# Kernel optimization log

Measured on AMD Instinct MI355X. Metric: run time of the kernel, lower is better.

Reference implementation:

```python
import jax, jax.numpy as jnp
import numpy as np

B, D, OUT, K = 2048, 256, 256, 16


def setup_inputs() -> dict:
    key = jax.random.key(0)
    k1, k2, k3, k4 = jax.random.split(key, 4)
    x = jax.random.normal(k1, (B, D), dtype=jnp.float32)
    values = jax.random.uniform(k2, (OUT, D, K), dtype=jnp.float32, minval=-0.05, maxval=0.05)
    skip_w = jax.random.normal(k3, (OUT, D), dtype=jnp.float32) * (1.0 / np.sqrt(D).astype(np.float32))
    skip_b = jax.random.normal(k4, (OUT,), dtype=jnp.float32) * 0.01
    return {"x": x, "values": values, "skip_w": skip_w, "skip_b": skip_b}


def reference(x, values, skip_w, skip_b):
    # x: (B, D); values: (OUT, D, K); skip_w: (OUT, D); skip_b: (OUT,)
    num_knots = values.shape[-1]
    grid = jnp.linspace(-1.0, 1.0, num_knots)  # (K,)
    xc = jnp.clip(x, -1.0, 1.0)
    # torch.bucketize(x, grid) with right=False == searchsorted side='left'
    right = jnp.searchsorted(grid, xc, side='left')
    left = jnp.clip(right - 1, 0, num_knots - 2)  # (B, D)
    right = left + 1
    g0 = grid[left]
    g1 = grid[right]
    w = (xc - g0) / (g1 - g0 + 1e-12)  # (B, D)
    # Gather spline values per (sample, input-dim) knot bucket.
    vt = jnp.transpose(values, (1, 2, 0))  # (D, K, OUT)
    dim_idx = jnp.arange(xc.shape[1])[None, :]  # (1, D)
    v_left = vt[dim_idx, left]    # (B, D, OUT)
    v_right = vt[dim_idx, right]  # (B, D, OUT)
    # Linear interpolation + sum over input dims.
    y = jnp.sum((1.0 - w)[..., None] * v_left + w[..., None] * v_right, axis=1)  # (B, OUT)
    # Skip connection on the clamped input (torch reassigns x = clamp(x) first).
    return y + xc @ skip_w.T + skip_b
```

## Files before the change

### kernel.cpp

```cpp
#include <hip/hip_runtime.h>
#include <hip/hip_bf16.h>


namespace {
constexpr int Bsz  = 2048;
constexpr int Din  = 256;
constexpr int Dout = 256;
constexpr int Kn   = 16;
constexpr int KKNOT = Din * Kn;
constexpr int Ksp   = KKNOT + Din;
constexpr int KB    = Ksp / 32;
constexpr int KBK   = KKNOT / 32;
constexpr float INV_H = 7.5f;
constexpr float Hgrid = 2.0f / 15.0f;

constexpr int NSPLIT = 9;
constexpr int STK    = 8;
constexpr int STS    = 4;
constexpr int PELEM  = Bsz * Dout;
constexpr int SXS    = 36;
}

typedef __attribute__((ext_vector_type(8))) short shortx8;
typedef __attribute__((ext_vector_type(4))) float floatx4;

__device__ __forceinline__ unsigned int f2bf(float f) {
  __hip_bfloat16 h = __float2bfloat16(f);
  return (unsigned int)*reinterpret_cast<unsigned short*>(&h);
}
__device__ __forceinline__ float clamp1(float v) {
  return fminf(1.f, fmaxf(-1.f, v));
}
__device__ __forceinline__ unsigned int packbf(unsigned int e0, unsigned int e1) {
  return (e1 & 0xffff0000u) | (e0 >> 16);
}
__device__ __forceinline__ unsigned int rnd(float f) {
  return __float_as_uint(f) + 0x8000u;
}

__global__ __launch_bounds__(256) void kan_prep(
    const float* __restrict__ values, const float* __restrict__ skip_w,
    unsigned short* __restrict__ Wf) {
  const int tid = blockIdx.x * 256 + threadIdx.x;
  const int q  = tid & 3;
  const int n  = (tid >> 2) & 15;
  const int og = (tid >> 6) & 15;
  const int kb = tid >> 10;
  const int o  = og * 16 + n;
  const int k0 = kb * 32 + q * 8;
  const float* src = (kb < KBK)
      ? values + (size_t)o * KKNOT + k0
      : skip_w + (size_t)o * Din + (k0 - KKNOT);
  const float4 v0 = *(const float4*)src;
  const float4 v1 = *(const float4*)(src + 4);
  const size_t chunk = (size_t)kb * 1024 + og * 64 + q * 16 + n;
  *(uint4*)(Wf + chunk * 8) = make_uint4(
      f2bf(v0.x) | (f2bf(v0.y) << 16), f2bf(v0.z) | (f2bf(v0.w) << 16),
      f2bf(v1.x) | (f2bf(v1.y) << 16), f2bf(v1.z) | (f2bf(v1.w) << 16));
}

__global__ __launch_bounds__(256) void kan_gemm(
    const float* __restrict__ x, const unsigned short* __restrict__ Wf,
    float* __restrict__ part) {
  __shared__ float sx[32 * SXS];
  __shared__ __align__(16) unsigned short aLds[2][32 * 64];

  const int tid  = threadIdx.x;
  const int wave = tid >> 6, lane = tid & 63;
  const int ks   = blockIdx.x % NSPLIT;
  const int mi   = blockIdx.x / NSPLIT;
  const int m0   = mi * 32;
  const int og0  = wave * 4;
  const int lrow = lane & 15, lq = lane >> 4;

  const int brow = tid >> 3;
  const int bseg = tid & 7;
  const int kbi  = bseg >> 2;
  const int dsel = (bseg >> 1) & 1;
  const float h0 = (float)((bseg & 1) * 8);

  const uint4* B = (const uint4*)Wf;

  floatx4 acc[2][4] = {};
  uint4 bb[2][8];

  if (ks < 8) {
    const int kb0 = ks * 16;
    const int d0  = ks * 32;
    {
      const float4 v = *(const float4*)(x + (size_t)(m0 + brow) * Din + d0 + bseg * 4);
      *(float4*)&sx[brow * SXS + bseg * 4] = v;
    }
    __syncthreads();

    #pragma unroll
    for (int kk = 0; kk < 2; ++kk)
      #pragma unroll
      for (int j = 0; j < 4; ++j)
        bb[0][kk * 4 + j] = B[(size_t)(kb0 + kk) * 1024 + (og0 + j) * 64 + lane];
    {
      const float xv = sx[brow * SXS + 2 * kbi + dsel];
      const float t  = (clamp1(xv) + 1.f) * INV_H;
      unsigned int e[8];
      #pragma unroll
      for (int h = 0; h < 8; ++h)
        e[h] = rnd(fmaxf(0.f, 1.f - fabsf(t - (h0 + (float)h))));
      *(uint4*)&aLds[0][brow * 64 + bseg * 8] =
          make_uint4(packbf(e[0], e[1]), packbf(e[2], e[3]),
                     packbf(e[4], e[5]), packbf(e[6], e[7]));
    }

    for (int s = 0; s < STK; ++s) {
      const int cur = s & 1, nxt = cur ^ 1;
      if (s + 1 < STK) {
        #pragma unroll
        for (int kk = 0; kk < 2; ++kk)
          #pragma unroll
          for (int j = 0; j < 4; ++j)
            bb[nxt][kk * 4 + j] =
                B[(size_t)(kb0 + 2 * (s + 1) + kk) * 1024 + (og0 + j) * 64 + lane];
      }
      __syncthreads();

      if (s + 1 < STK) {
        const float xv = sx[brow * SXS + 4 * (s + 1) + 2 * kbi + dsel];
        const float t  = (clamp1(xv) + 1.f) * INV_H;
        unsigned int e[8];
        #pragma unroll
        for (int h = 0; h < 8; ++h)
          e[h] = rnd(fmaxf(0.f, 1.f - fabsf(t - (h0 + (float)h))));
        *(uint4*)&aLds[nxt][brow * 64 + bseg * 8] =
            make_uint4(packbf(e[0], e[1]), packbf(e[2], e[3]),
                       packbf(e[4], e[5]), packbf(e[6], e[7]));
      }

      shortx8 af[2][2];
      #pragma unroll
      for (int i = 0; i < 2; ++i)
        #pragma unroll
        for (int kk = 0; kk < 2; ++kk)
          af[i][kk] = *(const shortx8*)&aLds[cur][(16 * i + lrow) * 64 + kk * 32 + lq * 8];
      #pragma unroll
      for (int kk = 0; kk < 2; ++kk)
        #pragma unroll
        for (int j = 0; j < 4; ++j) {
          union { uint4 u; shortx8 s; } bc;
          bc.u = bb[cur][kk * 4 + j];
          #pragma unroll
          for (int i = 0; i < 2; ++i)
            acc[i][j] = __builtin_amdgcn_mfma_f32_16x16x32_bf16(af[i][kk], bc.s, acc[i][j], 0, 0, 0);
        }
    }
  } else {
    const int kb0 = KBK;
    const float* xrow = x + (size_t)(m0 + brow) * Din;
    float4 pxa[2], pxb[2];
    #pragma unroll
    for (int kk = 0; kk < 2; ++kk)
      #pragma unroll
      for (int j = 0; j < 4; ++j)
        bb[0][kk * 4 + j] = B[(size_t)(kb0 + kk) * 1024 + (og0 + j) * 64 + lane];
    pxa[0] = *(const float4*)(xrow + bseg * 8);
    pxb[0] = *(const float4*)(xrow + bseg * 8 + 4);
    {
      unsigned int e[8];
      e[0] = rnd(clamp1(pxa[0].x)); e[1] = rnd(clamp1(pxa[0].y));
      e[2] = rnd(clamp1(pxa[0].z)); e[3] = rnd(clamp1(pxa[0].w));
      e[4] = rnd(clamp1(pxb[0].x)); e[5] = rnd(clamp1(pxb[0].y));
      e[6] = rnd(clamp1(pxb[0].z)); e[7] = rnd(clamp1(pxb[0].w));
      *(uint4*)&aLds[0][brow * 64 + bseg * 8] =
          make_uint4(packbf(e[0], e[1]), packbf(e[2], e[3]),
                     packbf(e[4], e[5]), packbf(e[6], e[7]));
    }

    for (int s = 0; s < STS; ++s) {
      const int cur = s & 1, nxt = cur ^ 1;
      if (s + 1 < STS) {
        #pragma unroll
        for (int kk = 0; kk < 2; ++kk)
          #pragma unroll
          for (int j = 0; j < 4; ++j)
            bb[nxt][kk * 4 + j] =
                B[(size_t)(kb0 + 2 * (s + 1) + kk) * 1024 + (og0 + j) * 64 + lane];
        pxa[nxt] = *(const float4*)(xrow + (s + 1) * 64 + bseg * 8);
        pxb[nxt] = *(const float4*)(xrow + (s + 1) * 64 + bseg * 8 + 4);
      }
      __syncthreads();

      if (s + 1 < STS) {
        unsigned int e[8];
        e[0] = rnd(clamp1(pxa[nxt].x)); e[1] = rnd(clamp1(pxa[nxt].y));
        e[2] = rnd(clamp1(pxa[nxt].z)); e[3] = rnd(clamp1(pxa[nxt].w));
        e[4] = rnd(clamp1(pxb[nxt].x)); e[5] = rnd(clamp1(pxb[nxt].y));
        e[6] = rnd(clamp1(pxb[nxt].z)); e[7] = rnd(clamp1(pxb[nxt].w));
        *(uint4*)&aLds[nxt][brow * 64 + bseg * 8] =
            make_uint4(packbf(e[0], e[1]), packbf(e[2], e[3]),
                       packbf(e[4], e[5]), packbf(e[6], e[7]));
      }

      shortx8 af[2][2];
      #pragma unroll
      for (int i = 0; i < 2; ++i)
        #pragma unroll
        for (int kk = 0; kk < 2; ++kk)
          af[i][kk] = *(const shortx8*)&aLds[cur][(16 * i + lrow) * 64 + kk * 32 + lq * 8];
      #pragma unroll
      for (int kk = 0; kk < 2; ++kk)
        #pragma unroll
        for (int j = 0; j < 4; ++j) {
          union { uint4 u; shortx8 s; } bc;
          bc.u = bb[cur][kk * 4 + j];
          #pragma unroll
          for (int i = 0; i < 2; ++i)
            acc[i][j] = __builtin_amdgcn_mfma_f32_16x16x32_bf16(af[i][kk], bc.s, acc[i][j], 0, 0, 0);
        }
    }
  }

  const int wtile = mi * 4 + wave;
  float* P = part + (size_t)ks * PELEM + (size_t)wtile * 2048;
  #pragma unroll
  for (int i = 0; i < 2; ++i)
    #pragma unroll
    for (int j = 0; j < 4; ++j)
      *(floatx4*)&P[((i * 4 + j) * 64 + lane) * 4] = acc[i][j];
}

__global__ __launch_bounds__(256) void kan_reduce(
    const float* __restrict__ part, const float* __restrict__ skip_b,
    float* __restrict__ out) {
  const int tid = blockIdx.x * 256 + threadIdx.x;
  float4 a = make_float4(0.f, 0.f, 0.f, 0.f);
  #pragma unroll
  for (int s = 0; s < NSPLIT; ++s) {
    const float4 p = *(const float4*)(part + (size_t)s * PELEM + (size_t)tid * 4);
    a.x += p.x; a.y += p.y; a.z += p.z; a.w += p.w;
  }
  const int f4    = tid & 511, wtile = tid >> 9;
  const int ij    = f4 >> 6,  lane  = f4 & 63;
  const int i     = ij >> 2,  j     = ij & 3;
  const int mi    = wtile >> 2;
  const int wave  = wtile & 3;
  const int b0    = mi * 32 + 16 * i + (lane >> 4) * 4;
  const int o     = wave * 64 + 16 * j + (lane & 15);
  const float sb  = skip_b[o];
  out[(size_t)(b0 + 0) * Dout + o] = a.x + sb;
  out[(size_t)(b0 + 1) * Dout + o] = a.y + sb;
  out[(size_t)(b0 + 2) * Dout + o] = a.z + sb;
  out[(size_t)(b0 + 3) * Dout + o] = a.w + sb;
}

__device__ __forceinline__ void knot_interp(float xraw, float& xv, float& w, int& l) {
  xv = fminf(1.0f, fmaxf(-1.0f, xraw));
  float t = (xv + 1.0f) * INV_H;
  l = (int)ceilf(t) - 1;
  l = l < 0 ? 0 : (l > Kn - 2 ? Kn - 2 : l);
  float g0 = -1.0f + Hgrid * (float)l;
  w = (xv - g0) * INV_H;
}

__global__ __launch_bounds__(256) void prep_transpose(
    const float* __restrict__ values, const float* __restrict__ skip_w,
    float* __restrict__ vt, float* __restrict__ swt) {
  int idx = blockIdx.x * blockDim.x + threadIdx.x;
  if (idx < Din * Kn * Dout) {
    int k = idx & (Kn - 1);
    int d = (idx >> 4) & (Din - 1);
    int o = idx >> 12;
    vt[(d * Kn + k) * Dout + o] = values[idx];
  }
  if (idx < Dout * Din) {
    int d = idx & (Din - 1);
    int o = idx >> 8;
    swt[d * Dout + o] = skip_w[idx];
  }
}

__global__ __launch_bounds__(256) void kan_main(
    const float* __restrict__ x, const float* __restrict__ vt,
    const float* __restrict__ swt, const float* __restrict__ skip_b,
    float* __restrict__ out) {
  __shared__ float s_w[4][Din];
  __shared__ float s_x[4][Din];
  __shared__ int   s_l[4][Din];
  const int tid = threadIdx.x;
  const int b0  = blockIdx.x * 4;
  for (int i = tid; i < 4 * Din; i += 256) {
    int bb = i >> 8;
    int d  = i & (Din - 1);
    float xv, w; int l;
    knot_interp(x[(b0 + bb) * Din + d], xv, w, l);
    s_w[bb][d] = w; s_x[bb][d] = xv; s_l[bb][d] = l;
  }
  __syncthreads();
  const int g = tid >> 6, lane = tid & 63;
  const int o = lane << 2, b = b0 + g;
  float4 acc = make_float4(0.f, 0.f, 0.f, 0.f);
  for (int d = 0; d < Din; ++d) {
    const float w = s_w[g][d], xv = s_x[g][d];
    const int l = s_l[g][d];
    const float* base = vt + (d * Kn + l) * Dout + o;
    const float4 vl = *(const float4*)(base);
    const float4 vr = *(const float4*)(base + Dout);
    const float4 sw = *(const float4*)(swt + d * Dout + o);
    acc.x = fmaf(xv, sw.x, fmaf(w, vr.x - vl.x, acc.x + vl.x));
    acc.y = fmaf(xv, sw.y, fmaf(w, vr.y - vl.y, acc.y + vl.y));
    acc.z = fmaf(xv, sw.z, fmaf(w, vr.z - vl.z, acc.z + vl.z));
    acc.w = fmaf(xv, sw.w, fmaf(w, vr.w - vl.w, acc.w + vl.w));
  }
  const float4 bias = *(const float4*)(skip_b + o);
  acc.x += bias.x; acc.y += bias.y; acc.z += bias.z; acc.w += bias.w;
  *(float4*)(out + (size_t)b * Dout + o) = acc;
}

extern "C" void kernel_launch(void* const* d_in, const int* in_sizes, int n_in,
                              void* d_out, int out_size, void* d_ws, size_t ws_size,
                              hipStream_t stream) {
  (void)in_sizes; (void)n_in; (void)out_size;
  const float* x      = (const float*)d_in[0];
  const float* values = (const float*)d_in[1];
  const float* skip_w = (const float*)d_in[2];
  const float* skip_b = (const float*)d_in[3];
  float* out = (float*)d_out;

  const size_t wf_bytes   = (size_t)Dout * Ksp * sizeof(unsigned short);
  const size_t part_bytes = (size_t)NSPLIT * PELEM * sizeof(float);
  const size_t need_gemm  = wf_bytes + part_bytes;
  const size_t need_fb    = (size_t)(Din * Kn * Dout + Din * Dout) * sizeof(float);

  if (ws_size >= need_gemm) {
    unsigned short* Wf = (unsigned short*)d_ws;
    float* part = (float*)((char*)d_ws + wf_bytes);
    kan_prep<<<(KB * 1024) / 256, 256, 0, stream>>>(values, skip_w, Wf);
    kan_gemm<<<(Bsz / 32) * NSPLIT, 256, 0, stream>>>(x, Wf, part);
    kan_reduce<<<PELEM / 4 / 256, 256, 0, stream>>>(part, skip_b, out);
  } else if (ws_size >= need_fb) {
    float* vt  = (float*)d_ws;
    float* swt = vt + Din * Kn * Dout;
    prep_transpose<<<(Din * Kn * Dout + 255) / 256, 256, 0, stream>>>(values, skip_w, vt, swt);
    kan_main<<<Bsz / 4, 256, 0, stream>>>(x, vt, swt, skip_b, out);
  }
}
```

Before: 77.88 us.

## Fold skip weights into spline matrix and fuse split-K reduction into GEMM

After: 97.29 us. 24.9% more time.

```diff
diff --git a/kernel.cpp b/kernel.cpp
--- a/kernel.cpp
+++ b/kernel.cpp
@@ -8,16 +8,12 @@
 constexpr int Dout = 256;
 constexpr int Kn   = 16;
 constexpr int KKNOT = Din * Kn;
-constexpr int Ksp   = KKNOT + Din;
-constexpr int KB    = Ksp / 32;
-constexpr int KBK   = KKNOT / 32;
+constexpr int KB    = KKNOT / 32;
 constexpr float INV_H = 7.5f;
 constexpr float Hgrid = 2.0f / 15.0f;
 
-constexpr int NSPLIT = 9;
+constexpr int NSPLIT = 8;
 constexpr int STK    = 8;
-constexpr int STS    = 4;
-constexpr int PELEM  = Bsz * Dout;
 constexpr int SXS    = 36;
 }
 
@@ -40,7 +36,8 @@
 
 __global__ __launch_bounds__(256) void kan_prep(
     const float* __restrict__ values, const float* __restrict__ skip_w,
-    unsigned short* __restrict__ Wf) {
+    unsigned short* __restrict__ Wf, unsigned int* __restrict__ cnt) {
+  if (blockIdx.x == 0 && threadIdx.x < 64) cnt[threadIdx.x] = 0u;
   const int tid = blockIdx.x * 256 + threadIdx.x;
   const int q  = tid & 3;
   const int n  = (tid >> 2) & 15;
@@ -48,27 +45,34 @@
   const int kb = tid >> 10;
   const int o  = og * 16 + n;
   const int k0 = kb * 32 + q * 8;
-  const float* src = (kb < KBK)
-      ? values + (size_t)o * KKNOT + k0
-      : skip_w + (size_t)o * Din + (k0 - KKNOT);
+  const int d  = k0 >> 4;
+  const float h0 = (float)(k0 & 15);
+  const float sw = skip_w[o * Din + d];
+  const float* src = values + (size_t)o * KKNOT + k0;
   const float4 v0 = *(const float4*)src;
   const float4 v1 = *(const float4*)(src + 4);
+  float e[8] = {v0.x, v0.y, v0.z, v0.w, v1.x, v1.y, v1.z, v1.w};
+  #pragma unroll
+  for (int j = 0; j < 8; ++j)
+    e[j] = fmaf(-1.f + (h0 + (float)j) * Hgrid, sw, e[j]);
   const size_t chunk = (size_t)kb * 1024 + og * 64 + q * 16 + n;
   *(uint4*)(Wf + chunk * 8) = make_uint4(
-      f2bf(v0.x) | (f2bf(v0.y) << 16), f2bf(v0.z) | (f2bf(v0.w) << 16),
-      f2bf(v1.x) | (f2bf(v1.y) << 16), f2bf(v1.z) | (f2bf(v1.w) << 16));
+      f2bf(e[0]) | (f2bf(e[1]) << 16), f2bf(e[2]) | (f2bf(e[3]) << 16),
+      f2bf(e[4]) | (f2bf(e[5]) << 16), f2bf(e[6]) | (f2bf(e[7]) << 16));
 }
 
 __global__ __launch_bounds__(256) void kan_gemm(
     const float* __restrict__ x, const unsigned short* __restrict__ Wf,
-    float* __restrict__ part) {
+    const float* __restrict__ skip_b, float* __restrict__ part,
+    unsigned int* __restrict__ cnt, float* __restrict__ out) {
   __shared__ float sx[32 * SXS];
   __shared__ __align__(16) unsigned short aLds[2][32 * 64];
+  __shared__ int s_last;
 
   const int tid  = threadIdx.x;
   const int wave = tid >> 6, lane = tid & 63;
-  const int ks   = blockIdx.x % NSPLIT;
-  const int mi   = blockIdx.x / NSPLIT;
+  const int ks   = blockIdx.x >> 6;
+  const int mi   = blockIdx.x & 63;
   const int m0   = mi * 32;
   const int og0  = wave * 4;
   const int lrow = lane & 15, lq = lane >> 4;
@@ -84,170 +88,112 @@
   floatx4 acc[2][4] = {};
   uint4 bb[2][8];
 
-  if (ks < 8) {
-    const int kb0 = ks * 16;
-    const int d0  = ks * 32;
-    {
-      const float4 v = *(const float4*)(x + (size_t)(m0 + brow) * Din + d0 + bseg * 4);
-      *(float4*)&sx[brow * SXS + bseg * 4] = v;
+  const int kb0 = ks * 16;
+  const int d0  = ks * 32;
+  {
+    const float4 v = *(const float4*)(x + (size_t)(m0 + brow) * Din + d0 + bseg * 4);
+    *(float4*)&sx[brow * SXS + bseg * 4] = v;
+  }
+  __syncthreads();
+
+  #pragma unroll
+  for (int kk = 0; kk < 2; ++kk)
+    #pragma unroll
+    for (int j = 0; j < 4; ++j)
+      bb[0][kk * 4 + j] = B[(size_t)(kb0 + kk) * 1024 + (og0 + j) * 64 + lane];
+  {
+    const float xv = sx[brow * SXS + 2 * kbi + dsel];
+    const float t  = (clamp1(xv) + 1.f) * INV_H;
+    unsigned int e[8];
+    #pragma unroll
+    for (int h = 0; h < 8; ++h)
+      e[h] = rnd(fmaxf(0.f, 1.f - fabsf(t - (h0 + (float)h))));
+    *(uint4*)&aLds[0][brow * 64 + bseg * 8] =
+        make_uint4(packbf(e[0], e[1]), packbf(e[2], e[3]),
+                   packbf(e[4], e[5]), packbf(e[6], e[7]));
+  }
+
+  for (int s = 0; s < STK; ++s) {
+    const int cur = s & 1, nxt = cur ^ 1;
+    if (s + 1 < STK) {
+      #pragma unroll
+      for (int kk = 0; kk < 2; ++kk)
+        #pragma unroll
+        for (int j = 0; j < 4; ++j)
+          bb[nxt][kk * 4 + j] =
+              B[(size_t)(kb0 + 2 * (s + 1) + kk) * 1024 + (og0 + j) * 64 + lane];
     }
     __syncthreads();
 
-    #pragma unroll
-    for (int kk = 0; kk < 2; ++kk)
-      #pragma unroll
-      for (int j = 0; j < 4; ++j)
-        bb[0][kk * 4 + j] = B[(size_t)(kb0 + kk) * 1024 + (og0 + j) * 64 + lane];
-    {
-      const float xv = sx[brow * SXS + 2 * kbi + dsel];
+    if (s + 1 < STK) {
+      const float xv = sx[brow * SXS + 4 * (s + 1) + 2 * kbi + dsel];
       const float t  = (clamp1(xv) + 1.f) * INV_H;
       unsigned int e[8];
       #pragma unroll
       for (int h = 0; h < 8; ++h)
         e[h] = rnd(fmaxf(0.f, 1.f - fabsf(t - (h0 + (float)h))));
-      *(uint4*)&aLds[0][brow * 64 + bseg * 8] =
+      *(uint4*)&aLds[nxt][brow * 64 + bseg * 8] =
           make_uint4(packbf(e[0], e[1]), packbf(e[2], e[3]),
                      packbf(e[4], e[5]), packbf(e[6], e[7]));
     }
 
-    for (int s = 0; s < STK; ++s) {
-      const int cur = s & 1, nxt = cur ^ 1;
-      if (s + 1 < STK) {
+    shortx8 af[2][2];
+    #pragma unroll
+    for (int i = 0; i < 2; ++i)
+      #pragma unroll
+      for (int kk = 0; kk < 2; ++kk)
+        af[i][kk] = *(const shortx8*)&aLds[cur][(16 * i + lrow) * 64 + kk * 32 + lq * 8];
+    #pragma unroll
+    for (int kk = 0; kk < 2; ++kk)
+      #pragma unroll
+      for (int j = 0; j < 4; ++j) {
+        union { uint4 u; shortx8 s; } bc;
+        bc.u = bb[cur][kk * 4 + j];
         #pragma unroll
-        for (int kk = 0; kk < 2; ++kk)
-          #pragma unroll
-          for (int j = 0; j < 4; ++j)
-            bb[nxt][kk * 4 + j] =
-                B[(size_t)(kb0 + 2 * (s + 1) + kk) * 1024 + (og0 + j) * 64 + lane];
+        for (int i = 0; i < 2; ++i)
+          acc[i][j] = __builtin_amdgcn_mfma_f32_16x16x32_bf16(af[i][kk], bc.s, acc[i][j], 0, 0, 0);
       }
-      __syncthreads();
-
-      if (s + 1 < STK) {
-        const float xv = sx[brow * SXS + 4 * (s + 1) + 2 * kbi + dsel];
-        const float t  = (clamp1(xv) + 1.f) * INV_H;
-        unsigned int e[8];
-        #pragma unroll
-        for (int h = 0; h < 8; ++h)
-          e[h] = rnd(fmaxf(0.f, 1.f - fabsf(t - (h0 + (float)h))));
-        *(uint4*)&aLds[nxt][brow * 64 + bseg * 8] =
-            make_uint4(packbf(e[0], e[1]), packbf(e[2], e[3]),
-                       packbf(e[4], e[5]), packbf(e[6], e[7]));
-      }
-
-      shortx8 af[2][2];
-      #pragma unroll
-      for (int i = 0; i < 2; ++i)
-        #pragma unroll
-        for (int kk = 0; kk < 2; ++kk)
-          af[i][kk] = *(const shortx8*)&aLds[cur][(16 * i + lrow) * 64 + kk * 32 + lq * 8];
-      #pragma unroll
-      for (int kk = 0; kk < 2; ++kk)
-        #pragma unroll
-        for (int j = 0; j < 4; ++j) {
-          union { uint4 u; shortx8 s; } bc;
-          bc.u = bb[cur][kk * 4 + j];
-          #pragma unroll
-          for (int i = 0; i < 2; ++i)
-            acc[i][j] = __builtin_amdgcn_mfma_f32_16x16x32_bf16(af[i][kk], bc.s, acc[i][j], 0, 0, 0);
-        }
-    }
-  } else {
-    const int kb0 = KBK;
-    const float* xrow = x + (size_t)(m0 + brow) * Din;
-    float4 pxa[2], pxb[2];
-    #pragma unroll
-    for (int kk = 0; kk < 2; ++kk)
-      #pragma unroll
-      for (int j = 0; j < 4; ++j)
-        bb[0][kk * 4 + j] = B[(size_t)(kb0 + kk) * 1024 + (og0 + j) * 64 + lane];
-    pxa[0] = *(const float4*)(xrow + bseg * 8);
-    pxb[0] = *(const float4*)(xrow + bseg * 8 + 4);
-    {
-      unsigned int e[8];
-      e[0] = rnd(clamp1(pxa[0].x)); e[1] = rnd(clamp1(pxa[0].y));
-      e[2] = rnd(clamp1(pxa[0].z)); e[3] = rnd(clamp1(pxa[0].w));
-      e[4] = rnd(clamp1(pxb[0].x)); e[5] = rnd(clamp1(pxb[0].y));
-      e[6] = rnd(clamp1(pxb[0].z)); e[7] = rnd(clamp1(pxb[0].w));
-      *(uint4*)&aLds[0][brow * 64 + bseg * 8] =
-          make_uint4(packbf(e[0], e[1]), packbf(e[2], e[3]),
-                     packbf(e[4], e[5]), packbf(e[6], e[7]));
-    }
-
-    for (int s = 0; s < STS; ++s) {
-      const int cur = s & 1, nxt = cur ^ 1;
-      if (s + 1 < STS) {
-        #pragma unroll
-        for (int kk = 0; kk < 2; ++kk)
-          #pragma unroll
-          for (int j = 0; j < 4; ++j)
-            bb[nxt][kk * 4 + j] =
-                B[(size_t)(kb0 + 2 * (s + 1) + kk) * 1024 + (og0 + j) * 64 + lane];
-        pxa[nxt] = *(const float4*)(xrow + (s + 1) * 64 + bseg * 8);
-        pxb[nxt] = *(const float4*)(xrow + (s + 1) * 64 + bseg * 8 + 4);
-      }
-      __syncthreads();
-
-      if (s + 1 < STS) {
-        unsigned int e[8];
-        e[0] = rnd(clamp1(pxa[nxt].x)); e[1] = rnd(clamp1(pxa[nxt].y));
-        e[2] = rnd(clamp1(pxa[nxt].z)); e[3] = rnd(clamp1(pxa[nxt].w));
-        e[4] = rnd(clamp1(pxb[nxt].x)); e[5] = rnd(clamp1(pxb[nxt].y));
-        e[6] = rnd(clamp1(pxb[nxt].z)); e[7] = rnd(clamp1(pxb[nxt].w));
-        *(uint4*)&aLds[nxt][brow * 64 + bseg * 8] =
-            make_uint4(packbf(e[0], e[1]), packbf(e[2], e[3]),
-                       packbf(e[4], e[5]), packbf(e[6], e[7]));
-      }
-
-      shortx8 af[2][2];
-      #pragma unroll
-      for (int i = 0; i < 2; ++i)
-        #pragma unroll
-        for (int kk = 0; kk < 2; ++kk)
-          af[i][kk] = *(const shortx8*)&aLds[cur][(16 * i + lrow) * 64 + kk * 32 + lq * 8];
-      #pragma unroll
-      for (int kk = 0; kk < 2; ++kk)
-        #pragma unroll
-        for (int j = 0; j < 4; ++j) {
-          union { uint4 u; shortx8 s; } bc;
-          bc.u = bb[cur][kk * 4 + j];
-          #pragma unroll
-          for (int i = 0; i < 2; ++i)
-            acc[i][j] = __builtin_amdgcn_mfma_f32_16x16x32_bf16(af[i][kk], bc.s, acc[i][j], 0, 0, 0);
-        }
-    }
-  }
-
-  const int wtile = mi * 4 + wave;
-  float* P = part + (size_t)ks * PELEM + (size_t)wtile * 2048;
+  }
+
+  float4* P4 = (float4*)part;
+  const size_t sbase = ((size_t)mi * NSPLIT + ks) * 2048 + wave * 512;
   #pragma unroll
   for (int i = 0; i < 2; ++i)
     #pragma unroll
     for (int j = 0; j < 4; ++j)
-      *(floatx4*)&P[((i * 4 + j) * 64 + lane) * 4] = acc[i][j];
-}
-
-__global__ __launch_bounds__(256) void kan_reduce(
-    const float* __restrict__ part, const float* __restrict__ skip_b,
-    float* __restrict__ out) {
-  const int tid = blockIdx.x * 256 + threadIdx.x;
-  float4 a = make_float4(0.f, 0.f, 0.f, 0.f);
-  #pragma unroll
-  for (int s = 0; s < NSPLIT; ++s) {
-    const float4 p = *(const float4*)(part + (size_t)s * PELEM + (size_t)tid * 4);
-    a.x += p.x; a.y += p.y; a.z += p.z; a.w += p.w;
-  }
-  const int f4    = tid & 511, wtile = tid >> 9;
-  const int ij    = f4 >> 6,  lane  = f4 & 63;
-  const int i     = ij >> 2,  j     = ij & 3;
-  const int mi    = wtile >> 2;
-  const int wave  = wtile & 3;
-  const int b0    = mi * 32 + 16 * i + (lane >> 4) * 4;
-  const int o     = wave * 64 + 16 * j + (lane & 15);
-  const float sb  = skip_b[o];
-  out[(size_t)(b0 + 0) * Dout + o] = a.x + sb;
-  out[(size_t)(b0 + 1) * Dout + o] = a.y + sb;
-  out[(size_t)(b0 + 2) * Dout + o] = a.z + sb;
-  out[(size_t)(b0 + 3) * Dout + o] = a.w + sb;
+      P4[sbase + (i * 4 + j) * 64 + lane] =
+          make_float4(acc[i][j][0], acc[i][j][1], acc[i][j][2], acc[i][j][3]);
+  __syncthreads();
+
+  if (tid == 0) {
+    unsigned int old = __hip_atomic_fetch_add(&cnt[mi], 1u, __ATOMIC_ACQ_REL,
+                                              __HIP_MEMORY_SCOPE_AGENT);
+    s_last = (old == NSPLIT - 1);
+  }
+  __syncthreads();
+  if (s_last) {
+    const float4* Pm = (const float4*)part + (size_t)mi * NSPLIT * 2048;
+    #pragma unroll
+    for (int p = 0; p < 8; ++p) {
+      const int g = p * 256 + tid;
+      float4 a = Pm[g];
+      #pragma unroll
+      for (int sp = 1; sp < NSPLIT; ++sp) {
+        const float4 b = Pm[sp * 2048 + g];
+        a.x += b.x; a.y += b.y; a.z += b.z; a.w += b.w;
+      }
+      const int w  = g >> 9, qq = g & 511;
+      const int ij = qq >> 6, ln = qq & 63;
+      const int i  = ij >> 2, j = ij & 3;
+      const int b0 = mi * 32 + 16 * i + ((ln >> 4) << 2);
+      const int o  = w * 64 + 16 * j + (ln & 15);
+      const float sb = skip_b[o];
+      out[(size_t)(b0 + 0) * Dout + o] = a.x + sb;
+      out[(size_t)(b0 + 1) * Dout + o] = a.y + sb;
+      out[(size_t)(b0 + 2) * Dout + o] = a.z + sb;
+      out[(size_t)(b0 + 3) * Dout + o] = a.w + sb;
+    }
+  }
 }
 
 __device__ __forceinline__ void knot_interp(float xraw, float& xv, float& w, int& l) {
@@ -323,17 +269,18 @@
   const float* skip_b = (const float*)d_in[3];
   float* out = (float*)d_out;
 
-  const size_t wf_bytes   = (size_t)Dout * Ksp * sizeof(unsigned short);
-  const size_t part_bytes = (size_t)NSPLIT * PELEM * sizeof(float);
-  const size_t need_gemm  = wf_bytes + part_bytes;
+  const size_t wf_bytes   = (size_t)Dout * KKNOT * sizeof(unsigned short);
+  const size_t cnt_bytes  = 256;
+  const size_t part_bytes = (size_t)64 * NSPLIT * 8192 * sizeof(float);
+  const size_t need_gemm  = wf_bytes + cnt_bytes + part_bytes;
   const size_t need_fb    = (size_t)(Din * Kn * Dout + Din * Dout) * sizeof(float);
 
   if (ws_size >= need_gemm) {
     unsigned short* Wf = (unsigned short*)d_ws;
-    float* part = (float*)((char*)d_ws + wf_bytes);
-    kan_prep<<<(KB * 1024) / 256, 256, 0, stream>>>(values, skip_w, Wf);
-    kan_gemm<<<(Bsz / 32) * NSPLIT, 256, 0, stream>>>(x, Wf, part);
-    kan_reduce<<<PELEM / 4 / 256, 256, 0, stream>>>(part, skip_b, out);
+    unsigned int* cnt  = (unsigned int*)((char*)d_ws + wf_bytes);
+    float* part        = (float*)((char*)d_ws + wf_bytes + cnt_bytes);
+    kan_prep<<<(KB * 1024) / 256, 256, 0, stream>>>(values, skip_w, Wf, cnt);
+    kan_gemm<<<64 * NSPLIT, 256, 0, stream>>>(x, Wf, skip_b, part, cnt, out);
   } else if (ws_size >= need_fb) {
     float* vt  = (float*)d_ws;
     float* swt = vt + Din * Kn * Dout;
```
